# Performance work log

Hardware: AMD Instinct MI355X
Metric: run time of the kernel (lower is better)

## Reference

```python
import jax, jax.numpy as jnp
import numpy as np

C = 256; G = 16; GC = C // G; K = 3; P = K * K
N = 4; H = 64; W = 64
PAD = 1; OFFSET_SCALE = 1.0; LN_EPS = 1e-5


def setup_inputs() -> dict:
    key = jax.random.key(0)
    ks = jax.random.split(key, 8)
    s = 0.02
    return {
        "x": jax.random.normal(ks[0], (N, C, H, W), jnp.float32),
        "dw_w": jax.random.normal(ks[1], (C, 1, K, K), jnp.float32) * s,
        "dw_b": jnp.zeros((C,), jnp.float32),
        "ln_g": jnp.ones((C,), jnp.float32),
        "ln_b": jnp.zeros((C,), jnp.float32),
        "off_w": jax.random.normal(ks[2], (C, G * P * 2), jnp.float32) * s,
        "off_b": jnp.zeros((G * P * 2,), jnp.float32),
        "mask_w": jax.random.normal(ks[3], (C, G * P), jnp.float32) * s,
        "mask_b": jnp.zeros((G * P,), jnp.float32),
        "inp_w": jax.random.normal(ks[4], (C, C), jnp.float32) * s,
        "inp_b": jnp.zeros((C,), jnp.float32),
        "out_w": jax.random.normal(ks[5], (C, C), jnp.float32) * s,
        "out_b": jnp.zeros((C,), jnp.float32),
    }


def _dcnv3_nchw(x, dw_w, dw_b, ln_g, ln_b, off_w, off_b, mask_w, mask_b,
                inp_w, inp_b, out_w, out_b):
    # NCHW -> NHWC (wrapper permute)
    xn = jnp.transpose(x, (0, 2, 3, 1))                      # (N,H,W,C)
    x_proj = xn @ inp_w + inp_b                              # input_proj

    # offset/mask branch: depthwise conv (NCHW) -> LayerNorm (channels-last) -> GELU
    x1 = jax.lax.conv_general_dilated(
        x, dw_w, window_strides=(1, 1), padding=((PAD, PAD), (PAD, PAD)),
        dimension_numbers=("NCHW", "OIHW", "NCHW"), feature_group_count=C)
    x1 = jnp.transpose(x1, (0, 2, 3, 1)) + dw_b
    mu = x1.mean(-1, keepdims=True)
    var = ((x1 - mu) ** 2).mean(-1, keepdims=True)
    x1 = (x1 - mu) * jax.lax.rsqrt(var + LN_EPS) * ln_g + ln_b
    x1 = jax.nn.gelu(x1, approximate=False)

    offset = (x1 @ off_w + off_b).reshape(N, H, W, G, P, 2)  # (x,y) pairs
    mask = jax.nn.softmax((x1 @ mask_w + mask_b).reshape(N, H, W, G, P), axis=-1)

    # pad sampled feature map with zeros (F.pad before sampling)
    xp = jnp.pad(x_proj, ((0, 0), (PAD, PAD), (PAD, PAD), (0, 0)))
    Hin, Win = H + 2 * PAD, W + 2 * PAD
    xg = xp.reshape(N, Hin, Win, G, GC)

    # reference points, normalized by padded size
    ref_y = (jnp.arange(H, dtype=jnp.float32) + PAD + 0.5) / Hin
    ref_x = (jnp.arange(W, dtype=jnp.float32) + PAD + 0.5) / Win
    ref = jnp.stack([jnp.broadcast_to(ref_x[None, :], (H, W)),
                     jnp.broadcast_to(ref_y[:, None], (H, W))], -1)  # (H,W,2)

    # dilation grid: x varies in the outer loop (torch meshgrid 'ij')
    d = jnp.arange(K, dtype=jnp.float32) - (K - 1) // 2     # [-1,0,1]
    gx = jnp.repeat(d, K) / Win
    gy = jnp.tile(d, K) / Hin
    grid = jnp.stack([gx, gy], -1)                           # (P,2)

    norm = jnp.array([Win, Hin], jnp.float32)
    loc = (ref[None, :, :, None, None, :] + grid * OFFSET_SCALE
           + offset * OFFSET_SCALE / norm)                   # (N,H,W,G,P,2)

    # grid_sample bilinear, align_corners=False, zero padding
    px = loc[..., 0] * Win - 0.5
    py = loc[..., 1] * Hin - 0.5
    x0 = jnp.floor(px); y0 = jnp.floor(py)
    wx = px - x0; wy = py - y0
    x0i = x0.astype(jnp.int32); y0i = y0.astype(jnp.int32)

    n_idx = jnp.arange(N)[:, None, None, None, None]
    g_idx = jnp.arange(G)[None, None, None, :, None]

    def corner(iy, ix, w):
        valid = (iy >= 0) & (iy < Hin) & (ix >= 0) & (ix < Win)
        v = xg[n_idx, jnp.clip(iy, 0, Hin - 1), jnp.clip(ix, 0, Win - 1), g_idx]
        wgt = jnp.where(valid, w, 0.0) * mask                # fold mask into weights
        return jnp.einsum("nhwgp,nhwgpc->nhwgc", wgt, v)

    out = (corner(y0i, x0i, (1 - wy) * (1 - wx))
           + corner(y0i, x0i + 1, (1 - wy) * wx)
           + corner(y0i + 1, x0i, wy * (1 - wx))
           + corner(y0i + 1, x0i + 1, wy * wx))               # (N,H,W,G,GC)

    out = out.reshape(N, H, W, C) @ out_w + out_b            # output_proj
    return jnp.transpose(out, (0, 3, 1, 2))                  # NHWC -> NCHW


def reference(x, dw_w, dw_b, ln_g, ln_b, off_w, off_b, mask_w, mask_b,
              inp_w, inp_b, out_w, out_b):
    return _dcnv3_nchw(x, dw_w, dw_b, ln_g, ln_b, off_w, off_b,
                       mask_w, mask_b, inp_w, inp_b, out_w, out_b)
```

## Files before the change

### kernel.cpp

```cpp
#include <hip/hip_runtime.h>
#include <hip/hip_bf16.h>
#include <math.h>


using bf16x8 = __attribute__((ext_vector_type(8))) short;
using f32x4  = __attribute__((ext_vector_type(4))) float;

#define GLOBAL_AS __attribute__((address_space(1)))
#define LDS_AS    __attribute__((address_space(3)))

static __device__ inline void g2lds16(const void* g, void* l) {
  __builtin_amdgcn_global_load_lds((const GLOBAL_AS int*)g, (LDS_AS int*)l, 16, 0, 0);
}
static __device__ inline unsigned short f2bf(float v) {
  __hip_bfloat16 b = __float2bfloat16(v);
  return *reinterpret_cast<unsigned short*>(&b);
}
static __device__ inline float us2f(unsigned short u) {
  union { unsigned u; float f; } c; c.u = ((unsigned)u) << 16; return c.f;
}

__global__ __launch_bounds__(256) void prep_k(
    const float* __restrict__ inp_w, const float* __restrict__ off_w,
    const float* __restrict__ off_b, const float* __restrict__ mask_w,
    const float* __restrict__ mask_b, const float* __restrict__ out_w,
    __hip_bfloat16* __restrict__ BtI, __hip_bfloat16* __restrict__ BtOM,
    __hip_bfloat16* __restrict__ BtO, float* __restrict__ bOM)
{
  int b = blockIdx.x, t = threadIdx.x;
  if (b < 256) {
    int n = b;
    BtI[n * 256 + t] = __float2bfloat16(inp_w[t * 256 + n]);
  } else if (b < 768) {
    int n = b - 256;
    float v = 0.f;
    if (n < 288) v = off_w[t * 288 + n];
    else if (n < 432) v = mask_w[t * 144 + (n - 288)];
    BtOM[n * 256 + t] = __float2bfloat16(v);
    if (b == 256) {
      for (int idx = t; idx < 512; idx += 256) {
        float bv = (idx < 288) ? off_b[idx] : ((idx < 432) ? mask_b[idx - 288] : 0.f);
        bOM[idx] = bv;
      }
    }
  } else {
    int n = b - 768;
    BtO[n * 256 + t] = __float2bfloat16(out_w[t * 256 + n]);
  }
}

__global__ __launch_bounds__(256) void xt_k(const float* __restrict__ x,
                                            __hip_bfloat16* __restrict__ xT) {
  __shared__ float tile[32][65];
  const int hw0 = blockIdx.x * 64, c0 = blockIdx.y * 32, n4 = blockIdx.z;
  const int t = threadIdx.x;
  #pragma unroll
  for (int r = 0; r < 8; ++r) {
    int idx = t + r * 256;
    int cl = idx >> 6, wl = idx & 63;
    tile[cl][wl] = x[(size_t)n4 * 1048576 + (size_t)(c0 + cl) * 4096 + hw0 + wl];
  }
  __syncthreads();
  #pragma unroll
  for (int r = 0; r < 2; ++r) {
    int idx = t + r * 256;
    int pixl = idx >> 3, cq = idx & 7;
    unsigned short b0 = f2bf(tile[cq * 4 + 0][pixl]);
    unsigned short b1 = f2bf(tile[cq * 4 + 1][pixl]);
    unsigned short b2 = f2bf(tile[cq * 4 + 2][pixl]);
    unsigned short b3 = f2bf(tile[cq * 4 + 3][pixl]);
    uint2 u;
    u.x = (unsigned)b0 | ((unsigned)b1 << 16);
    u.y = (unsigned)b2 | ((unsigned)b3 << 16);
    *(uint2*)&xT[((size_t)n4 * 4096 + hw0 + pixl) * 256 + c0 + cq * 4] = u;
  }
}

struct G64 {
  f32x4 acc[2][2];
  int wave, lane, quad, lr, wm, wn;
};

static __device__ inline void g64_loop(
    G64& g, const __hip_bfloat16* __restrict__ A,
    const __hip_bfloat16* __restrict__ Bt, size_t m0, int n0,
    short* As, short* Bs, int t)
{
  #pragma unroll
  for (int i = 0; i < 2; ++i)
    #pragma unroll
    for (int j = 0; j < 2; ++j)
      g.acc[i][j] = (f32x4){0.f, 0.f, 0.f, 0.f};
  const int row = t >> 2, kq = t & 3;
  for (int kt = 0; kt < 256; kt += 32) {
    g2lds16(A + (m0 + row) * 256 + kt + kq * 8, (char*)As + t * 16);
    g2lds16(Bt + (size_t)(n0 + row) * 256 + kt + kq * 8, (char*)Bs + t * 16);
    __syncthreads();
    bf16x8 bfv[2];
    #pragma unroll
    for (int ni = 0; ni < 2; ++ni)
      bfv[ni] = *(const bf16x8*)&Bs[(g.wn * 32 + ni * 16 + g.lr) * 32 + g.quad * 8];
    #pragma unroll
    for (int mi = 0; mi < 2; ++mi) {
      bf16x8 af = *(const bf16x8*)&As[(g.wm * 32 + mi * 16 + g.lr) * 32 + g.quad * 8];
      #pragma unroll
      for (int ni = 0; ni < 2; ++ni)
        g.acc[mi][ni] = __builtin_amdgcn_mfma_f32_16x16x32_bf16(af, bfv[ni], g.acc[mi][ni], 0, 0, 0);
    }
    __syncthreads();
  }
}

__global__ __launch_bounds__(256) void gemm_iom(
    const __hip_bfloat16* __restrict__ xT, const __hip_bfloat16* __restrict__ x1,
    const __hip_bfloat16* __restrict__ BtI, const __hip_bfloat16* __restrict__ BtOM,
    const float* __restrict__ inp_b, const float* __restrict__ bOM,
    __hip_bfloat16* __restrict__ xpu, __hip_bfloat16* __restrict__ om)
{
  __shared__ __align__(16) char smem[8192];
  short* As = (short*)smem;
  short* Bs = (short*)(smem + 4096);
  const int t = threadIdx.x;
  const int bx = blockIdx.x;
  const size_t m0 = (size_t)blockIdx.y * 64;

  const __hip_bfloat16* A;  const __hip_bfloat16* Bt;
  const float* bias;        __hip_bfloat16* C;
  int ldc, nst, n0;
  if (bx < 4) { A = xT; Bt = BtI;  bias = inp_b; C = xpu; ldc = 256; nst = 256; n0 = bx * 64; }
  else        { A = x1; Bt = BtOM; bias = bOM;   C = om;  ldc = 448; nst = 432; n0 = (bx - 4) * 64; }

  G64 g;
  g.wave = t >> 6; g.lane = t & 63; g.quad = g.lane >> 4; g.lr = g.lane & 15;
  g.wm = g.wave >> 1; g.wn = g.wave & 1;
  g64_loop(g, A, Bt, m0, n0, As, Bs, t);

  #pragma unroll
  for (int mi = 0; mi < 2; ++mi) {
    #pragma unroll
    for (int ni = 0; ni < 2; ++ni) {
      int col = n0 + g.wn * 32 + ni * 16 + g.lr;
      if (col < nst) {
        float bv = bias[col];
        #pragma unroll
        for (int reg = 0; reg < 4; ++reg) {
          size_t m = m0 + g.wm * 32 + mi * 16 + g.quad * 4 + reg;
          C[m * ldc + col] = __float2bfloat16(g.acc[mi][ni][reg] + bv);
        }
      }
    }
  }
}

__global__ __launch_bounds__(256) void gemm_o(
    const __hip_bfloat16* __restrict__ samp, const __hip_bfloat16* __restrict__ BtO,
    const float* __restrict__ out_b, float* __restrict__ out)
{
  __shared__ __align__(16) char smem[8448];
  short* As = (short*)smem;
  short* Bs = (short*)(smem + 4096);
  float* tb = (float*)smem;
  const int t = threadIdx.x;
  const int n0 = blockIdx.x * 64;
  const size_t m0 = (size_t)blockIdx.y * 64;

  G64 g;
  g.wave = t >> 6; g.lane = t & 63; g.quad = g.lane >> 4; g.lr = g.lane & 15;
  g.wm = g.wave >> 1; g.wn = g.wave & 1;
  g64_loop(g, samp, BtO, m0, n0, As, Bs, t);

  const int n4 = (int)(m0 >> 12), hw0 = (int)(m0 & 4095);
  for (int qc = 0; qc < 2; ++qc) {
    __syncthreads();
    if (g.wn == qc) {
      #pragma unroll
      for (int ni = 0; ni < 2; ++ni) {
        int cl = ni * 16 + g.lr;
        float bv = out_b[n0 + qc * 32 + cl];
        #pragma unroll
        for (int mi = 0; mi < 2; ++mi)
          #pragma unroll
          for (int reg = 0; reg < 4; ++reg)
            tb[cl * 65 + g.wm * 32 + mi * 16 + g.quad * 4 + reg] =
                g.acc[mi][ni][reg] + bv;
      }
    }
    __syncthreads();
    #pragma unroll
    for (int r = 0; r < 2; ++r) {
      int idx = t + r * 256;
      int row = idx >> 4, mc = (idx & 15) * 4;
      int co = n0 + qc * 32 + row;
      float4 v;
      v.x = tb[row * 65 + mc + 0];
      v.y = tb[row * 65 + mc + 1];
      v.z = tb[row * 65 + mc + 2];
      v.w = tb[row * 65 + mc + 3];
      *(float4*)&out[(size_t)(n4 * 256 + co) * 4096 + hw0 + mc] = v;
    }
  }
}

__global__ __launch_bounds__(256) void dwconv_k(
    const float* __restrict__ x, const float* __restrict__ dw_w,
    const float* __restrict__ dw_b, __hip_bfloat16* __restrict__ y)
{
  __shared__ float pl[4096];
  const int bc = blockIdx.x;
  const int n4 = bc >> 8, c = bc & 255;
  const int t = threadIdx.x;
  const float* xc = x + (size_t)n4 * 1048576 + (size_t)c * 4096;
  #pragma unroll
  for (int r = 0; r < 4; ++r) {
    int idx4 = t + r * 256;
    *(float4*)&pl[idx4 * 4] = *(const float4*)&xc[idx4 * 4];
  }
  float wv[9];
  #pragma unroll
  for (int i = 0; i < 9; ++i) wv[i] = dw_w[c * 9 + i];
  const float bb = dw_b[c];
  __syncthreads();
  __hip_bfloat16* yc = y + (size_t)(n4 * 256 + c) * 4096;
  #pragma unroll 4
  for (int r = 0; r < 16; ++r) {
    int px = t + r * 256;
    int h = px >> 6, w = px & 63;
    float s = bb;
    #pragma unroll
    for (int dh = -1; dh <= 1; ++dh) {
      int hh = h + dh;
      if ((unsigned)hh >= 64u) continue;
      #pragma unroll
      for (int dw = -1; dw <= 1; ++dw) {
        int ww = w + dw;
        if ((unsigned)ww >= 64u) continue;
        s = fmaf(pl[hh * 64 + ww], wv[(dh + 1) * 3 + (dw + 1)], s);
      }
    }
    yc[px] = __float2bfloat16(s);
  }
}

__global__ __launch_bounds__(1024) void ln_k(
    const __hip_bfloat16* __restrict__ y, const float* __restrict__ ln_g,
    const float* __restrict__ ln_b, __hip_bfloat16* __restrict__ x1)
{
  __shared__ unsigned short ys[256 * 66];
  __shared__ float gs[256], bs2[256];
  __shared__ float ps[16][64], pq[16][64], mu_s[64], rs_s[64];
  const int blk = blockIdx.x;
  const int n4 = blk >> 6, h = blk & 63;
  const int t = threadIdx.x;

  if (t < 256) { gs[t] = ln_g[t]; bs2[t] = ln_b[t]; }

  const __hip_bfloat16* yb = y + (size_t)n4 * 1048576 + h * 64;
  #pragma unroll
  for (int r = 0; r < 2; ++r) {
    int idx = t + r * 1024;
    int c = idx >> 3, w8 = idx & 7;
    uint4 u = *(const uint4*)(yb + (size_t)c * 4096 + w8 * 8);
    unsigned* d = (unsigned*)&ys[c * 66 + w8 * 8];
    d[0] = u.x; d[1] = u.y; d[2] = u.z; d[3] = u.w;
  }
  __syncthreads();

  const int w = t & 63, q = t >> 6;
  {
    float s1 = 0.f, s2 = 0.f;
    #pragma unroll
    for (int i = 0; i < 16; ++i) {
      float v = us2f(ys[(q * 16 + i) * 66 + w]);
      s1 += v; s2 = fmaf(v, v, s2);
    }
    ps[q][w] = s1; pq[q][w] = s2;
  }
  __syncthreads();
  if (t < 64) {
    float a = 0.f, b = 0.f;
    #pragma unroll
    for (int j = 0; j < 16; ++j) { a += ps[j][t]; b += pq[j][t]; }
    float mu = a * (1.f / 256.f);
    mu_s[t] = mu;
    rs_s[t] = rsqrtf(b * (1.f / 256.f) - mu * mu + 1e-5f);
  }
  __syncthreads();

  const float mu = mu_s[w], rs = rs_s[w];
  #pragma unroll
  for (int i = 0; i < 16; ++i) {
    int c = q * 16 + i;
    float v = us2f(ys[c * 66 + w]);
    float yv = fmaf((v - mu) * rs, gs[c], bs2[c]);
    float ge = 0.5f * yv * (1.f + erff(yv * 0.70710678f));
    ys[c * 66 + w] = f2bf(ge);
  }
  __syncthreads();

  const size_t row0 = ((size_t)n4 * 4096 + (size_t)h * 64) * 256;
  #pragma unroll
  for (int r = 0; r < 2; ++r) {
    int idx = t + r * 1024;
    int pix = idx >> 5, co8 = idx & 31;
    unsigned short v0 = ys[(co8 * 8 + 0) * 66 + pix];
    unsigned short v1 = ys[(co8 * 8 + 1) * 66 + pix];
    unsigned short v2 = ys[(co8 * 8 + 2) * 66 + pix];
    unsigned short v3 = ys[(co8 * 8 + 3) * 66 + pix];
    unsigned short v4 = ys[(co8 * 8 + 4) * 66 + pix];
    unsigned short v5 = ys[(co8 * 8 + 5) * 66 + pix];
    unsigned short v6 = ys[(co8 * 8 + 6) * 66 + pix];
    unsigned short v7 = ys[(co8 * 8 + 7) * 66 + pix];
    uint4 u;
    u.x = (unsigned)v0 | ((unsigned)v1 << 16);
    u.y = (unsigned)v2 | ((unsigned)v3 << 16);
    u.z = (unsigned)v4 | ((unsigned)v5 << 16);
    u.w = (unsigned)v6 | ((unsigned)v7 << 16);
    *(uint4*)&x1[row0 + (size_t)pix * 256 + co8 * 8] = u;
  }
}

__global__ __launch_bounds__(256) void sample_k(
    const __hip_bfloat16* __restrict__ xpu, const __hip_bfloat16* __restrict__ om,
    __hip_bfloat16* __restrict__ samp)
{
  __shared__ unsigned short oms[16 * 448];
  const int bid = blockIdx.x;
  const int region = bid & 7;
  const int q = bid >> 3;
  const int pix0 = region * 2048 + q * 16;
  const int t = threadIdx.x;

  {
    const uint4* gsrc = (const uint4*)(om + (size_t)pix0 * 448);
    uint4* ldst = (uint4*)oms;
    #pragma unroll
    for (int r = 0; r < 4; ++r) {
      int i = t + r * 256;
      if (i < 896) ldst[i] = gsrc[i];
    }
  }
  __syncthreads();

  const int g = t & 15;
  const int pl = t >> 4;
  const int pix = pix0 + pl;
  const int n4 = pix >> 12;
  const int hw = pix & 4095;
  const int h = hw >> 6, w = hw & 63;

  float mk[9];
  {
    const unsigned short* mp = &oms[pl * 448 + 288 + g * 9];
    float mx = -1e30f;
    #pragma unroll
    for (int p = 0; p < 9; ++p) { mk[p] = us2f(mp[p]); mx = fmaxf(mx, mk[p]); }
    float se = 0.f;
    #pragma unroll
    for (int p = 0; p < 9; ++p) { mk[p] = __expf(mk[p] - mx); se += mk[p]; }
    float inv = 1.f / se;
    #pragma unroll
    for (int p = 0; p < 9; ++p) mk[p] *= inv;
  }

  const unsigned short* op = &oms[pl * 448 + g * 18];
  const __hip_bfloat16* xpg = xpu + (g << 4);
  float ax[16];
  #pragma unroll
  for (int i = 0; i < 16; ++i) ax[i] = 0.f;

  auto corner = [&](int iy, int ix, float wt) {
    if ((unsigned)(iy - 1) >= 64u || (unsigned)(ix - 1) >= 64u) return;
    const __hip_bfloat16* src =
        xpg + ((size_t)((n4 << 12) + (iy - 1) * 64 + (ix - 1)) << 8);
    uint4 u0 = *(const uint4*)src;
    uint4 u1 = *(const uint4*)(src + 8);
    const unsigned uu[8] = {u0.x, u0.y, u0.z, u0.w, u1.x, u1.y, u1.z, u1.w};
    #pragma unroll
    for (int i = 0; i < 8; ++i) {
      float lo = us2f((unsigned short)(uu[i] & 0xffff));
      float hi = us2f((unsigned short)(uu[i] >> 16));
      ax[2 * i + 0] = fmaf(wt, lo, ax[2 * i + 0]);
      ax[2 * i + 1] = fmaf(wt, hi, ax[2 * i + 1]);
    }
  };

  #pragma unroll
  for (int p = 0; p < 9; ++p) {
    float ox = us2f(op[2 * p]), oy = us2f(op[2 * p + 1]);
    float px = (float)(w + p / 3) + ox;
    float py = (float)(h + p % 3) + oy;
    float xf = floorf(px), yf = floorf(py);
    float wx = px - xf, wy = py - yf;
    int ix = (int)xf, iy = (int)yf;
    float m = mk[p];
    corner(iy,     ix,     (1.f - wy) * (1.f - wx) * m);
    corner(iy,     ix + 1, (1.f - wy) * wx * m);
    corner(iy + 1, ix,     wy * (1.f - wx) * m);
    corner(iy + 1, ix + 1, wy * wx * m);
  }

  unsigned short ub[16];
  #pragma unroll
  for (int i = 0; i < 16; ++i) ub[i] = f2bf(ax[i]);
  uint4* d4 = (uint4*)(samp + (size_t)pix * 256 + (g << 4));
  uint4 u0, u1;
  u0.x = (unsigned)ub[0] | ((unsigned)ub[1] << 16);
  u0.y = (unsigned)ub[2] | ((unsigned)ub[3] << 16);
  u0.z = (unsigned)ub[4] | ((unsigned)ub[5] << 16);
  u0.w = (unsigned)ub[6] | ((unsigned)ub[7] << 16);
  u1.x = (unsigned)ub[8] | ((unsigned)ub[9] << 16);
  u1.y = (unsigned)ub[10] | ((unsigned)ub[11] << 16);
  u1.z = (unsigned)ub[12] | ((unsigned)ub[13] << 16);
  u1.w = (unsigned)ub[14] | ((unsigned)ub[15] << 16);
  d4[0] = u0; d4[1] = u1;
}

extern "C" void kernel_launch(void* const* d_in, const int* in_sizes, int n_in,
                              void* d_out, int out_size, void* d_ws, size_t ws_size,
                              hipStream_t stream) {
  const float* x      = (const float*)d_in[0];
  const float* dw_w   = (const float*)d_in[1];
  const float* dw_b   = (const float*)d_in[2];
  const float* ln_g   = (const float*)d_in[3];
  const float* ln_b   = (const float*)d_in[4];
  const float* off_w  = (const float*)d_in[5];
  const float* off_b  = (const float*)d_in[6];
  const float* mask_w = (const float*)d_in[7];
  const float* mask_b = (const float*)d_in[8];
  const float* inp_w  = (const float*)d_in[9];
  const float* inp_b  = (const float*)d_in[10];
  const float* out_w  = (const float*)d_in[11];
  const float* out_b  = (const float*)d_in[12];
  float* out = (float*)d_out;

  char* w0 = (char*)d_ws;
  __hip_bfloat16* xpu  = (__hip_bfloat16*)(w0);
  __hip_bfloat16* y    = (__hip_bfloat16*)(w0 + 8388608);
  __hip_bfloat16* x1   = (__hip_bfloat16*)(w0 + 16777216);
  __hip_bfloat16* xT   = (__hip_bfloat16*)(w0 + 25165824);
  __hip_bfloat16* samp = xT;
  __hip_bfloat16* om   = (__hip_bfloat16*)(w0 + 33554432);
  __hip_bfloat16* BtI  = (__hip_bfloat16*)(w0 + 48234496);
  __hip_bfloat16* BtOM = (__hip_bfloat16*)(w0 + 48365568);
  __hip_bfloat16* BtO  = (__hip_bfloat16*)(w0 + 48627712);
  float*          bOM  = (float*)(w0 + 48758784);
  if (ws_size < 48760832) return;

  prep_k<<<1024, 256, 0, stream>>>(inp_w, off_w, off_b, mask_w, mask_b, out_w,
                                   BtI, BtOM, BtO, bOM);
  xt_k<<<dim3(64, 8, 4), 256, 0, stream>>>(x, xT);
  dwconv_k<<<1024, 256, 0, stream>>>(x, dw_w, dw_b, y);
  ln_k<<<256, 1024, 0, stream>>>(y, ln_g, ln_b, x1);
  gemm_iom<<<dim3(11, 256), 256, 0, stream>>>(xT, x1, BtI, BtOM, inp_b, bOM, xpu, om);
  sample_k<<<1024, 256, 0, stream>>>(xpu, om, samp);
  gemm_o<<<dim3(4, 256), 256, 0, stream>>>(samp, BtO, out_b, out);
}
```

Before: 168.7 us.

## Fuse depthwise conv, LayerNorm, GELU and offset/mask GEMM into one kernel

Merges weight prep and the x transpose into a single launch. Replaces the separate dwconv, LayerNorm and combined GEMM kernels with one per-row kernel that computes the depthwise conv from the bf16 channels-last xT, normalizes and applies GELU in LDS, then runs the offset/mask MFMA GEMM straight from LDS. The input projection becomes its own GEMM kernel. This removes the y and x1 round trips through global memory and two launches, at the cost of a large-LDS 1024-thread block with only 256 blocks, and the conv now reads bf16-rounded input rather than fp32.

After: 163.3 us. 3.1% less time.

```diff
diff --git a/kernel.cpp b/kernel.cpp
--- a/kernel.cpp
+++ b/kernel.cpp
@@ -20,40 +20,41 @@
   union { unsigned u; float f; } c; c.u = ((unsigned)u) << 16; return c.f;
 }
 
-__global__ __launch_bounds__(256) void prep_k(
+__global__ __launch_bounds__(256) void prep_xt_k(
+    const float* __restrict__ x,
     const float* __restrict__ inp_w, const float* __restrict__ off_w,
     const float* __restrict__ off_b, const float* __restrict__ mask_w,
     const float* __restrict__ mask_b, const float* __restrict__ out_w,
     __hip_bfloat16* __restrict__ BtI, __hip_bfloat16* __restrict__ BtOM,
-    __hip_bfloat16* __restrict__ BtO, float* __restrict__ bOM)
-{
-  int b = blockIdx.x, t = threadIdx.x;
-  if (b < 256) {
-    int n = b;
-    BtI[n * 256 + t] = __float2bfloat16(inp_w[t * 256 + n]);
-  } else if (b < 768) {
-    int n = b - 256;
-    float v = 0.f;
-    if (n < 288) v = off_w[t * 288 + n];
-    else if (n < 432) v = mask_w[t * 144 + (n - 288)];
-    BtOM[n * 256 + t] = __float2bfloat16(v);
-    if (b == 256) {
-      for (int idx = t; idx < 512; idx += 256) {
-        float bv = (idx < 288) ? off_b[idx] : ((idx < 432) ? mask_b[idx - 288] : 0.f);
-        bOM[idx] = bv;
-      }
-    }
-  } else {
-    int n = b - 768;
-    BtO[n * 256 + t] = __float2bfloat16(out_w[t * 256 + n]);
-  }
-}
-
-__global__ __launch_bounds__(256) void xt_k(const float* __restrict__ x,
-                                            __hip_bfloat16* __restrict__ xT) {
+    __hip_bfloat16* __restrict__ BtO, float* __restrict__ bOM,
+    __hip_bfloat16* __restrict__ xT)
+{
   __shared__ float tile[32][65];
-  const int hw0 = blockIdx.x * 64, c0 = blockIdx.y * 32, n4 = blockIdx.z;
-  const int t = threadIdx.x;
+  const int b = blockIdx.x, t = threadIdx.x;
+  if (b < 1024) {
+    if (b < 256) {
+      int n = b;
+      BtI[n * 256 + t] = __float2bfloat16(inp_w[t * 256 + n]);
+    } else if (b < 768) {
+      int n = b - 256;
+      float v = 0.f;
+      if (n < 288) v = off_w[t * 288 + n];
+      else if (n < 432) v = mask_w[t * 144 + (n - 288)];
+      BtOM[n * 256 + t] = __float2bfloat16(v);
+      if (b == 256) {
+        for (int idx = t; idx < 512; idx += 256) {
+          float bv = (idx < 288) ? off_b[idx] : ((idx < 432) ? mask_b[idx - 288] : 0.f);
+          bOM[idx] = bv;
+        }
+      }
+    } else {
+      int n = b - 768;
+      BtO[n * 256 + t] = __float2bfloat16(out_w[t * 256 + n]);
+    }
+    return;
+  }
+  const int i = b - 1024;
+  const int hw0 = (i & 63) * 64, c0 = ((i >> 6) & 7) * 32, n4 = i >> 9;
   #pragma unroll
   for (int r = 0; r < 8; ++r) {
     int idx = t + r * 256;
@@ -111,211 +112,164 @@
   }
 }
 
-__global__ __launch_bounds__(256) void gemm_iom(
-    const __hip_bfloat16* __restrict__ xT, const __hip_bfloat16* __restrict__ x1,
-    const __hip_bfloat16* __restrict__ BtI, const __hip_bfloat16* __restrict__ BtOM,
-    const float* __restrict__ inp_b, const float* __restrict__ bOM,
-    __hip_bfloat16* __restrict__ xpu, __hip_bfloat16* __restrict__ om)
+__global__ __launch_bounds__(256) void gemm_i(
+    const __hip_bfloat16* __restrict__ xT, const __hip_bfloat16* __restrict__ BtI,
+    const float* __restrict__ inp_b, __hip_bfloat16* __restrict__ xpu)
 {
   __shared__ __align__(16) char smem[8192];
   short* As = (short*)smem;
   short* Bs = (short*)(smem + 4096);
   const int t = threadIdx.x;
-  const int bx = blockIdx.x;
+  const int n0 = blockIdx.x * 64;
   const size_t m0 = (size_t)blockIdx.y * 64;
-
-  const __hip_bfloat16* A;  const __hip_bfloat16* Bt;
-  const float* bias;        __hip_bfloat16* C;
-  int ldc, nst, n0;
-  if (bx < 4) { A = xT; Bt = BtI;  bias = inp_b; C = xpu; ldc = 256; nst = 256; n0 = bx * 64; }
-  else        { A = x1; Bt = BtOM; bias = bOM;   C = om;  ldc = 448; nst = 432; n0 = (bx - 4) * 64; }
 
   G64 g;
   g.wave = t >> 6; g.lane = t & 63; g.quad = g.lane >> 4; g.lr = g.lane & 15;
   g.wm = g.wave >> 1; g.wn = g.wave & 1;
-  g64_loop(g, A, Bt, m0, n0, As, Bs, t);
+  g64_loop(g, xT, BtI, m0, n0, As, Bs, t);
 
   #pragma unroll
   for (int mi = 0; mi < 2; ++mi) {
     #pragma unroll
     for (int ni = 0; ni < 2; ++ni) {
       int col = n0 + g.wn * 32 + ni * 16 + g.lr;
-      if (col < nst) {
-        float bv = bias[col];
-        #pragma unroll
-        for (int reg = 0; reg < 4; ++reg) {
-          size_t m = m0 + g.wm * 32 + mi * 16 + g.quad * 4 + reg;
-          C[m * ldc + col] = __float2bfloat16(g.acc[mi][ni][reg] + bv);
-        }
-      }
-    }
-  }
-}
-
-__global__ __launch_bounds__(256) void gemm_o(
-    const __hip_bfloat16* __restrict__ samp, const __hip_bfloat16* __restrict__ BtO,
-    const float* __restrict__ out_b, float* __restrict__ out)
-{
-  __shared__ __align__(16) char smem[8448];
-  short* As = (short*)smem;
-  short* Bs = (short*)(smem + 4096);
-  float* tb = (float*)smem;
-  const int t = threadIdx.x;
-  const int n0 = blockIdx.x * 64;
-  const size_t m0 = (size_t)blockIdx.y * 64;
-
-  G64 g;
-  g.wave = t >> 6; g.lane = t & 63; g.quad = g.lane >> 4; g.lr = g.lane & 15;
-  g.wm = g.wave >> 1; g.wn = g.wave & 1;
-  g64_loop(g, samp, BtO, m0, n0, As, Bs, t);
-
-  const int n4 = (int)(m0 >> 12), hw0 = (int)(m0 & 4095);
-  for (int qc = 0; qc < 2; ++qc) {
-    __syncthreads();
-    if (g.wn == qc) {
+      float bv = inp_b[col];
       #pragma unroll
-      for (int ni = 0; ni < 2; ++ni) {
-        int cl = ni * 16 + g.lr;
-        float bv = out_b[n0 + qc * 32 + cl];
-        #pragma unroll
-        for (int mi = 0; mi < 2; ++mi)
-          #pragma unroll
-          for (int reg = 0; reg < 4; ++reg)
-            tb[cl * 65 + g.wm * 32 + mi * 16 + g.quad * 4 + reg] =
-                g.acc[mi][ni][reg] + bv;
-      }
-    }
-    __syncthreads();
-    #pragma unroll
-    for (int r = 0; r < 2; ++r) {
-      int idx = t + r * 256;
-      int row = idx >> 4, mc = (idx & 15) * 4;
-      int co = n0 + qc * 32 + row;
-      float4 v;
-      v.x = tb[row * 65 + mc + 0];
-      v.y = tb[row * 65 + mc + 1];
-      v.z = tb[row * 65 + mc + 2];
-      v.w = tb[row * 65 + mc + 3];
-      *(float4*)&out[(size_t)(n4 * 256 + co) * 4096 + hw0 + mc] = v;
-    }
-  }
-}
-
-__global__ __launch_bounds__(256) void dwconv_k(
-    const float* __restrict__ x, const float* __restrict__ dw_w,
-    const float* __restrict__ dw_b, __hip_bfloat16* __restrict__ y)
-{
-  __shared__ float pl[4096];
-  const int bc = blockIdx.x;
-  const int n4 = bc >> 8, c = bc & 255;
-  const int t = threadIdx.x;
-  const float* xc = x + (size_t)n4 * 1048576 + (size_t)c * 4096;
-  #pragma unroll
-  for (int r = 0; r < 4; ++r) {
-    int idx4 = t + r * 256;
-    *(float4*)&pl[idx4 * 4] = *(const float4*)&xc[idx4 * 4];
-  }
-  float wv[9];
-  #pragma unroll
-  for (int i = 0; i < 9; ++i) wv[i] = dw_w[c * 9 + i];
-  const float bb = dw_b[c];
-  __syncthreads();
-  __hip_bfloat16* yc = y + (size_t)(n4 * 256 + c) * 4096;
-  #pragma unroll 4
-  for (int r = 0; r < 16; ++r) {
-    int px = t + r * 256;
-    int h = px >> 6, w = px & 63;
-    float s = bb;
-    #pragma unroll
-    for (int dh = -1; dh <= 1; ++dh) {
-      int hh = h + dh;
-      if ((unsigned)hh >= 64u) continue;
-      #pragma unroll
-      for (int dw = -1; dw <= 1; ++dw) {
-        int ww = w + dw;
-        if ((unsigned)ww >= 64u) continue;
-        s = fmaf(pl[hh * 64 + ww], wv[(dh + 1) * 3 + (dw + 1)], s);
-      }
-    }
-    yc[px] = __float2bfloat16(s);
-  }
-}
-
-__global__ __launch_bounds__(1024) void ln_k(
-    const __hip_bfloat16* __restrict__ y, const float* __restrict__ ln_g,
-    const float* __restrict__ ln_b, __hip_bfloat16* __restrict__ x1)
-{
-  __shared__ unsigned short ys[256 * 66];
-  __shared__ float gs[256], bs2[256];
-  __shared__ float ps[16][64], pq[16][64], mu_s[64], rs_s[64];
+      for (int reg = 0; reg < 4; ++reg) {
+        size_t m = m0 + g.wm * 32 + mi * 16 + g.quad * 4 + reg;
+        xpu[m * 256 + col] = __float2bfloat16(g.acc[mi][ni][reg] + bv);
+      }
+    }
+  }
+}
+
+__global__ __launch_bounds__(1024) void stage2_k(
+    const __hip_bfloat16* __restrict__ xT,
+    const float* __restrict__ dw_w, const float* __restrict__ dw_b,
+    const float* __restrict__ ln_g, const float* __restrict__ ln_b,
+    const __hip_bfloat16* __restrict__ BtOM, const float* __restrict__ bOM,
+    __hip_bfloat16* __restrict__ om)
+{
+  __shared__ __align__(16) char smem[62464];
+  unsigned short* x1t = (unsigned short*)smem;
+  unsigned short* xs  = (unsigned short*)(smem + 33792);
+  float* wgt  = (float*)(smem + 33792 + 15360);
+  float* psq  = (float*)(smem + 33792 + 15360 + 1152);
+  float* murs = (float*)(smem + 33792 + 15360 + 1152 + 8192);
+  short* Bs   = (short*)(smem + 33792);
+
   const int blk = blockIdx.x;
   const int n4 = blk >> 6, h = blk & 63;
   const int t = threadIdx.x;
-
-  if (t < 256) { gs[t] = ln_g[t]; bs2[t] = ln_b[t]; }
-
-  const __hip_bfloat16* yb = y + (size_t)n4 * 1048576 + h * 64;
-  #pragma unroll
-  for (int r = 0; r < 2; ++r) {
-    int idx = t + r * 1024;
-    int c = idx >> 3, w8 = idx & 7;
-    uint4 u = *(const uint4*)(yb + (size_t)c * 4096 + w8 * 8);
-    unsigned* d = (unsigned*)&ys[c * 66 + w8 * 8];
-    d[0] = u.x; d[1] = u.y; d[2] = u.z; d[3] = u.w;
-  }
-  __syncthreads();
-
   const int w = t & 63, q = t >> 6;
-  {
-    float s1 = 0.f, s2 = 0.f;
-    #pragma unroll
-    for (int i = 0; i < 16; ++i) {
-      float v = us2f(ys[(q * 16 + i) * 66 + w]);
-      s1 += v; s2 = fmaf(v, v, s2);
-    }
-    ps[q][w] = s1; pq[q][w] = s2;
-  }
+
+  float s1 = 0.f, s2 = 0.f;
+  for (int chunk = 0; chunk < 8; ++chunk) {
+    const int ch0 = chunk * 32;
+    if (t < 768) {
+      int r = t >> 8, i = t & 255;
+      int px = i >> 2, cq = i & 3;
+      int hh = h + r - 1;
+      uint4 v = {0, 0, 0, 0};
+      if ((unsigned)hh < 64u)
+        v = *(const uint4*)(xT + ((size_t)n4 * 4096 + (size_t)hh * 64 + px) * 256 + ch0 + cq * 8);
+      *(uint4*)&xs[(r * 64 + px) * 40 + cq * 8] = v;
+    }
+    if (t < 288) {
+      int p = t >> 5, lc = t & 31;
+      wgt[p * 32 + lc] = dw_w[(ch0 + lc) * 9 + p];
+    }
+    __syncthreads();
+    {
+      int c = ch0 + 2 * q;
+      float a0 = dw_b[c], a1 = dw_b[c + 1];
+      #pragma unroll
+      for (int p = 0; p < 9; ++p) {
+        int dh = p / 3, dwd = p % 3 - 1;
+        int ww = w + dwd;
+        if ((unsigned)ww < 64u) {
+          unsigned xv = *(const unsigned*)&xs[(dh * 64 + ww) * 40 + 2 * q];
+          float wa = wgt[p * 32 + 2 * q], wb = wgt[p * 32 + 2 * q + 1];
+          a0 = fmaf(us2f((unsigned short)(xv & 0xffff)), wa, a0);
+          a1 = fmaf(us2f((unsigned short)(xv >> 16)), wb, a1);
+        }
+      }
+      s1 += a0 + a1;
+      s2 = fmaf(a0, a0, fmaf(a1, a1, s2));
+      unsigned pk = (unsigned)f2bf(a0) | ((unsigned)f2bf(a1) << 16);
+      *(unsigned*)&x1t[w * 264 + c] = pk;
+    }
+    __syncthreads();
+  }
+
+  psq[q * 64 + w] = s1;
+  psq[1024 + q * 64 + w] = s2;
   __syncthreads();
   if (t < 64) {
     float a = 0.f, b = 0.f;
     #pragma unroll
-    for (int j = 0; j < 16; ++j) { a += ps[j][t]; b += pq[j][t]; }
+    for (int j = 0; j < 16; ++j) { a += psq[j * 64 + t]; b += psq[1024 + j * 64 + t]; }
     float mu = a * (1.f / 256.f);
-    mu_s[t] = mu;
-    rs_s[t] = rsqrtf(b * (1.f / 256.f) - mu * mu + 1e-5f);
+    murs[t] = mu;
+    murs[64 + t] = rsqrtf(b * (1.f / 256.f) - mu * mu + 1e-5f);
   }
   __syncthreads();
-
-  const float mu = mu_s[w], rs = rs_s[w];
-  #pragma unroll
-  for (int i = 0; i < 16; ++i) {
-    int c = q * 16 + i;
-    float v = us2f(ys[c * 66 + w]);
-    float yv = fmaf((v - mu) * rs, gs[c], bs2[c]);
-    float ge = 0.5f * yv * (1.f + erff(yv * 0.70710678f));
-    ys[c * 66 + w] = f2bf(ge);
+  {
+    float mu = murs[w], rs = murs[64 + w];
+    #pragma unroll
+    for (int chunk = 0; chunk < 8; ++chunk) {
+      int c = chunk * 32 + 2 * q;
+      unsigned pk = *(const unsigned*)&x1t[w * 264 + c];
+      float v0 = us2f((unsigned short)(pk & 0xffff));
+      float v1 = us2f((unsigned short)(pk >> 16));
+      float y0 = fmaf((v0 - mu) * rs, ln_g[c], ln_b[c]);
+      float y1 = fmaf((v1 - mu) * rs, ln_g[c + 1], ln_b[c + 1]);
+      float g0 = 0.5f * y0 * (1.f + erff(y0 * 0.70710678f));
+      float g1 = 0.5f * y1 * (1.f + erff(y1 * 0.70710678f));
+      *(unsigned*)&x1t[w * 264 + c] = (unsigned)f2bf(g0) | ((unsigned)f2bf(g1) << 16);
+    }
   }
   __syncthreads();
 
-  const size_t row0 = ((size_t)n4 * 4096 + (size_t)h * 64) * 256;
-  #pragma unroll
-  for (int r = 0; r < 2; ++r) {
-    int idx = t + r * 1024;
-    int pix = idx >> 5, co8 = idx & 31;
-    unsigned short v0 = ys[(co8 * 8 + 0) * 66 + pix];
-    unsigned short v1 = ys[(co8 * 8 + 1) * 66 + pix];
-    unsigned short v2 = ys[(co8 * 8 + 2) * 66 + pix];
-    unsigned short v3 = ys[(co8 * 8 + 3) * 66 + pix];
-    unsigned short v4 = ys[(co8 * 8 + 4) * 66 + pix];
-    unsigned short v5 = ys[(co8 * 8 + 5) * 66 + pix];
-    unsigned short v6 = ys[(co8 * 8 + 6) * 66 + pix];
-    unsigned short v7 = ys[(co8 * 8 + 7) * 66 + pix];
-    uint4 u;
-    u.x = (unsigned)v0 | ((unsigned)v1 << 16);
-    u.y = (unsigned)v2 | ((unsigned)v3 << 16);
-    u.z = (unsigned)v4 | ((unsigned)v5 << 16);
-    u.w = (unsigned)v6 | ((unsigned)v7 << 16);
-    *(uint4*)&x1[row0 + (size_t)pix * 256 + co8 * 8] = u;
+  const int wave = t >> 6, lane = t & 63;
+  const int quad = lane >> 4, lr = lane & 15;
+  const int wm = wave >> 2, wn = wave & 3;
+  f32x4 acc[7];
+  #pragma unroll
+  for (int i = 0; i < 7; ++i) acc[i] = (f32x4){0.f, 0.f, 0.f, 0.f};
+
+  for (int kt = 0; kt < 256; kt += 32) {
+    __syncthreads();
+    {
+      int col = t >> 2, kq = t & 3;
+      g2lds16(BtOM + (size_t)col * 256 + kt + kq * 8, (char*)Bs + t * 16);
+      int j = t + 1024;
+      if (j < 1792) {
+        col = j >> 2; kq = j & 3;
+        g2lds16(BtOM + (size_t)col * 256 + kt + kq * 8, (char*)Bs + j * 16);
+      }
+    }
+    __syncthreads();
+    bf16x8 af = *(const bf16x8*)&x1t[(wm * 16 + lr) * 264 + kt + quad * 8];
+    #pragma unroll
+    for (int ni = 0; ni < 7; ++ni) {
+      bf16x8 bf = *(const bf16x8*)&Bs[(wn * 112 + ni * 16 + lr) * 32 + quad * 8];
+      acc[ni] = __builtin_amdgcn_mfma_f32_16x16x32_bf16(af, bf, acc[ni], 0, 0, 0);
+    }
+  }
+
+  const size_t pix0 = (size_t)n4 * 4096 + (size_t)h * 64;
+  #pragma unroll
+  for (int ni = 0; ni < 7; ++ni) {
+    int col = wn * 112 + ni * 16 + lr;
+    if (col < 432) {
+      float bv = bOM[col];
+      #pragma unroll
+      for (int reg = 0; reg < 4; ++reg) {
+        int m = wm * 16 + quad * 4 + reg;
+        om[(pix0 + m) * 448 + col] = __float2bfloat16(acc[ni][reg] + bv);
+      }
+    }
   }
 }
 
@@ -413,6 +367,55 @@
   u1.z = (unsigned)ub[12] | ((unsigned)ub[13] << 16);
   u1.w = (unsigned)ub[14] | ((unsigned)ub[15] << 16);
   d4[0] = u0; d4[1] = u1;
+}
+
+__global__ __launch_bounds__(256) void gemm_o(
+    const __hip_bfloat16* __restrict__ samp, const __hip_bfloat16* __restrict__ BtO,
+    const float* __restrict__ out_b, float* __restrict__ out)
+{
+  __shared__ __align__(16) char smem[8448];
+  short* As = (short*)smem;
+  short* Bs = (short*)(smem + 4096);
+  float* tb = (float*)smem;
+  const int t = threadIdx.x;
+  const int n0 = blockIdx.x * 64;
+  const size_t m0 = (size_t)blockIdx.y * 64;
+
+  G64 g;
+  g.wave = t >> 6; g.lane = t & 63; g.quad = g.lane >> 4; g.lr = g.lane & 15;
+  g.wm = g.wave >> 1; g.wn = g.wave & 1;
+  g64_loop(g, samp, BtO, m0, n0, As, Bs, t);
+
+  const int n4 = (int)(m0 >> 12), hw0 = (int)(m0 & 4095);
+  for (int qc = 0; qc < 2; ++qc) {
+    __syncthreads();
+    if (g.wn == qc) {
+      #pragma unroll
+      for (int ni = 0; ni < 2; ++ni) {
+        int cl = ni * 16 + g.lr;
+        float bv = out_b[n0 + qc * 32 + cl];
+        #pragma unroll
+        for (int mi = 0; mi < 2; ++mi)
+          #pragma unroll
+          for (int reg = 0; reg < 4; ++reg)
+            tb[cl * 65 + g.wm * 32 + mi * 16 + g.quad * 4 + reg] =
+                g.acc[mi][ni][reg] + bv;
+      }
+    }
+    __syncthreads();
+    #pragma unroll
+    for (int r = 0; r < 2; ++r) {
+      int idx = t + r * 256;
+      int row = idx >> 4, mc = (idx & 15) * 4;
+      int co = n0 + qc * 32 + row;
+      float4 v;
+      v.x = tb[row * 65 + mc + 0];
+      v.y = tb[row * 65 + mc + 1];
+      v.z = tb[row * 65 + mc + 2];
+      v.w = tb[row * 65 + mc + 3];
+      *(float4*)&out[(size_t)(n4 * 256 + co) * 4096 + hw0 + mc] = v;
+    }
+  }
 }
 
 extern "C" void kernel_launch(void* const* d_in, const int* in_sizes, int n_in,
@@ -435,23 +438,19 @@
 
   char* w0 = (char*)d_ws;
   __hip_bfloat16* xpu  = (__hip_bfloat16*)(w0);
-  __hip_bfloat16* y    = (__hip_bfloat16*)(w0 + 8388608);
-  __hip_bfloat16* x1   = (__hip_bfloat16*)(w0 + 16777216);
-  __hip_bfloat16* xT   = (__hip_bfloat16*)(w0 + 25165824);
+  __hip_bfloat16* xT   = (__hip_bfloat16*)(w0 + 8388608);
   __hip_bfloat16* samp = xT;
-  __hip_bfloat16* om   = (__hip_bfloat16*)(w0 + 33554432);
-  __hip_bfloat16* BtI  = (__hip_bfloat16*)(w0 + 48234496);
-  __hip_bfloat16* BtOM = (__hip_bfloat16*)(w0 + 48365568);
-  __hip_bfloat16* BtO  = (__hip_bfloat16*)(w0 + 48627712);
-  float*          bOM  = (float*)(w0 + 48758784);
-  if (ws_size < 48760832) return;
-
-  prep_k<<<1024, 256, 0, stream>>>(inp_w, off_w, off_b, mask_w, mask_b, out_w,
-                                   BtI, BtOM, BtO, bOM);
-  xt_k<<<dim3(64, 8, 4), 256, 0, stream>>>(x, xT);
-  dwconv_k<<<1024, 256, 0, stream>>>(x, dw_w, dw_b, y);
-  ln_k<<<256, 1024, 0, stream>>>(y, ln_g, ln_b, x1);
-  gemm_iom<<<dim3(11, 256), 256, 0, stream>>>(xT, x1, BtI, BtOM, inp_b, bOM, xpu, om);
+  __hip_bfloat16* om   = (__hip_bfloat16*)(w0 + 16777216);
+  __hip_bfloat16* BtI  = (__hip_bfloat16*)(w0 + 31457280);
+  __hip_bfloat16* BtOM = (__hip_bfloat16*)(w0 + 31588352);
+  __hip_bfloat16* BtO  = (__hip_bfloat16*)(w0 + 31850496);
+  float*          bOM  = (float*)(w0 + 31981568);
+  if (ws_size < 31983616) return;
+
+  prep_xt_k<<<3072, 256, 0, stream>>>(x, inp_w, off_w, off_b, mask_w, mask_b,
+                                      out_w, BtI, BtOM, BtO, bOM, xT);
+  gemm_i<<<dim3(4, 256), 256, 0, stream>>>(xT, BtI, inp_b, xpu);
+  stage2_k<<<256, 1024, 0, stream>>>(xT, dw_w, dw_b, ln_g, ln_b, BtOM, bOM, om);
   sample_k<<<1024, 256, 0, stream>>>(xpu, om, samp);
   gemm_o<<<dim3(4, 256), 256, 0, stream>>>(samp, BtO, out_b, out);
 }
```
